# Optimization experiments

Measured on AMD Instinct MI355X. Metric: run time of the kernel, lower is better.

## Reference

```python
import jax, jax.numpy as jnp
import numpy as np

HIDDEN = 2048
N_HEADS = 16
HEAD_DIM = HIDDEN // N_HEADS
ROPE_BASE = 10000.0


def rotate_half(x):
    half = x.shape[-1] // 2
    return jnp.concatenate((-x[..., half:], x[..., :half]), axis=-1)


def rope_cos_sin(seq_len, dtype):
    inv_freq = 1.0 / (ROPE_BASE ** (jnp.arange(0, HEAD_DIM, 2, dtype=jnp.float32) / HEAD_DIM))
    pos = jnp.arange(seq_len, dtype=jnp.float32)
    freqs = jnp.einsum('i,j->ij', pos, inv_freq)  # [S, hd/2]
    emb = jnp.concatenate((freqs, freqs), axis=-1)  # [S, hd]
    return jnp.cos(emb).astype(dtype), jnp.sin(emb).astype(dtype)


def setup_inputs() -> dict:
    key = jax.random.key(0)
    ks = jax.random.split(key, 9)
    B, S, H = 2, 2048, HIDDEN
    std = 1.0 / np.sqrt(H)
    return {
        'hidden_states': jax.random.normal(ks[0], (B, S, H), dtype=jnp.float32),
        'Wq': jax.random.uniform(ks[1], (H, H), jnp.float32, -std, std),
        'bq': jax.random.uniform(ks[2], (H,), jnp.float32, -std, std),
        'Wk': jax.random.uniform(ks[3], (H, H), jnp.float32, -std, std),
        'bk': jax.random.uniform(ks[4], (H,), jnp.float32, -std, std),
        'Wv': jax.random.uniform(ks[5], (H, H), jnp.float32, -std, std),
        'bv': jax.random.uniform(ks[6], (H,), jnp.float32, -std, std),
        'Wo': jax.random.uniform(ks[7], (H, H), jnp.float32, -std, std),
        'bo': jax.random.uniform(ks[8], (H,), jnp.float32, -std, std),
    }


def reference(hidden_states, Wq, bq, Wk, bk, Wv, bv, Wo, bo):
    B, S, H = hidden_states.shape
    scale = HEAD_DIM ** -0.5

    def proj(W, b):
        # torch Linear: x @ W.T + b
        y = jnp.einsum('bsh,oh->bso', hidden_states, W) + b
        return y.reshape(B, S, N_HEADS, HEAD_DIM).transpose(0, 2, 1, 3)  # [B,nh,S,hd]

    q = proj(Wq, bq)
    k = proj(Wk, bk)
    v = proj(Wv, bv)

    cos, sin = rope_cos_sin(S, hidden_states.dtype)  # [S, hd]
    cos = cos[None, None, :, :]
    sin = sin[None, None, :, :]
    q = q * cos + rotate_half(q) * sin
    k = k * cos + rotate_half(k) * sin

    scores = jnp.einsum('bhqd,bhkd->bhqk', q, k) * scale  # [B,nh,S,S]
    probs = jax.nn.softmax(scores, axis=-1)
    ctx = jnp.einsum('bhqk,bhkd->bhqd', probs, v)
    ctx = ctx.transpose(0, 2, 1, 3).reshape(B, S, H)
    return jnp.einsum('bsh,oh->bso', ctx, Wo) + bo
```

## Files before the change

kernel.cpp:

```cpp
#include <hip/hip_runtime.h>
#include <hip/hip_bf16.h>
#include <math.h>

#define HIDDEN 2048
#define NH 16
#define HD 128
#define NB 2
#define SEQ 2048
#define K_DIM 2048

typedef unsigned int u32;
typedef unsigned short ushort_t;
typedef __bf16 bf16x8 __attribute__((ext_vector_type(8)));
typedef float f32x4 __attribute__((ext_vector_type(4)));
typedef ushort_t u16x8 __attribute__((ext_vector_type(8)));

__device__ __forceinline__ void split1(float x, unsigned short& h, unsigned short& l) {
    u32 u = __float_as_uint(x);
    u32 hr = (u + 0x7FFFu + ((u >> 16) & 1u)) >> 16;
    h = (unsigned short)hr;
    float r = x - __uint_as_float(hr << 16);
    u32 u2 = __float_as_uint(r);
    l = (unsigned short)((u2 + 0x7FFFu + ((u2 >> 16) & 1u)) >> 16);
}

__device__ __forceinline__ ushort_t bf16r(float x) {
    u32 u = __float_as_uint(x);
    return (ushort_t)((u + 0x7FFFu + ((u >> 16) & 1u)) >> 16);
}

__device__ __forceinline__ void gl_lds16(const void* g, void* l) {
    __builtin_amdgcn_global_load_lds(
        (const __attribute__((address_space(1))) u32*)g,
        (__attribute__((address_space(3))) u32*)l, 16, 0, 0);
}

__global__ void k_rope_tables(float* __restrict__ ct, float* __restrict__ st) {
    int idx = blockIdx.x * 256 + threadIdx.x;
    int s = idx >> 6, d = idx & 63;
    double inv = pow(10000.0, -(double)d * (1.0 / 64.0));
    double ang = (double)s * inv;
    ct[idx] = (float)cos(ang);
    st[idx] = (float)sin(ang);
}

#define XG 2097152
#define WG 1048576
__global__ void k_cvt_all(const float4* __restrict__ X, const float4* __restrict__ W0,
                          const float4* __restrict__ W1, const float4* __restrict__ W2,
                          ushort4* __restrict__ Xh, ushort4* __restrict__ H0,
                          ushort4* __restrict__ H1, ushort4* __restrict__ H2) {
    int idx = blockIdx.x * 256 + threadIdx.x;
    const float4* src;
    ushort4* dst;
    int off;
    if (idx < XG) { src = X; dst = Xh; off = idx; }
    else {
        int t = idx - XG;
        int m = t >> 20;
        off = t & (WG - 1);
        src = (m == 0) ? W0 : (m == 1) ? W1 : W2;
        dst = (m == 0) ? H0 : (m == 1) ? H1 : H2;
    }
    float4 x = src[off];
    ushort4 h;
    h.x = bf16r(x.x); h.y = bf16r(x.y); h.z = bf16r(x.z); h.w = bf16r(x.w);
    dst[off] = h;
}

__global__ void k_split(const float4* __restrict__ src, ushort4* __restrict__ hi,
                        ushort4* __restrict__ lo) {
    int idx = blockIdx.x * 256 + threadIdx.x;
    float4 x = src[idx];
    ushort4 h, l;
    split1(x.x, h.x, l.x);
    split1(x.y, h.y, l.y);
    split1(x.z, h.z, l.z);
    split1(x.w, h.w, l.w);
    hi[idx] = h;
    lo[idx] = l;
}

#define BAR  __builtin_amdgcn_s_barrier()
#define VM6  asm volatile("s_waitcnt vmcnt(6)" ::: "memory")
#define VM4  asm volatile("s_waitcnt vmcnt(4)" ::: "memory")
#define VM0  asm volatile("s_waitcnt vmcnt(0)" ::: "memory")
#define PRIO1 __builtin_amdgcn_s_setprio(1)
#define PRIO0 __builtin_amdgcn_s_setprio(0)

#define QSTAGE(slot, kt) do { \
    const ushort_t* gA_ = Xh + sgA + (size_t)(kt) * 32; \
    gl_lds16(gA_, &As[slot][(w * 32) * 32]); \
    gl_lds16(gA_ + 16 * 2048, &As[slot][(w * 32 + 16) * 32]); \
    const ushort_t* gB_ = Wsel + sgB + (size_t)(kt) * 32; \
    gl_lds16(gB_, &Bs[slot][(w * 32) * 32]); \
    gl_lds16(gB_ + 16 * 2048, &Bs[slot][(w * 32 + 16) * 32]); \
} while (0)

#define QRD(AD, BD, slot) do { \
    _Pragma("unroll") for (int mf = 0; mf < 8; mf++) \
        AD[mf] = *(const bf16x8*)&As[slot][arow + mf * 512 + ccq]; \
    _Pragma("unroll") for (int nf = 0; nf < 4; nf++) \
        BD[nf] = *(const bf16x8*)&Bs[slot][brow + nf * 512 + ccq]; \
} while (0)

#define QMFMA(AD, BD) do { PRIO1; \
    _Pragma("unroll") for (int mf = 0; mf < 8; mf++) \
    _Pragma("unroll") for (int nf = 0; nf < 4; nf++) \
        acc[mf][nf] = __builtin_amdgcn_mfma_f32_16x16x32_bf16( \
            AD[mf], BD[nf], acc[mf][nf], 0, 0, 0); \
    PRIO0; } while (0)

__global__ __launch_bounds__(512, 2)
void k_gemm_qkv8(const ushort_t* __restrict__ Xh,
                 const ushort_t* __restrict__ W0, const ushort_t* __restrict__ W1,
                 const ushort_t* __restrict__ W2,
                 const float* __restrict__ b0, const float* __restrict__ b1,
                 const float* __restrict__ b2,
                 float* __restrict__ o0, float* __restrict__ o1, float* __restrict__ o2) {
    __shared__ ushort_t As[4][256 * 32];
    __shared__ ushort_t Bs[4][256 * 32];
    const int tid = threadIdx.x;
    const int lane = tid & 63;
    const int w = tid >> 6;
    const int wm = w >> 2;
    const int wn = w & 3;
    const int quad = lane >> 4;
    const int l15 = lane & 15;

    int bid = blockIdx.x;
    bid = (bid & 7) * 48 + (bid >> 3);
    const int bx = bid & 15;
    const int by = bid >> 4;
    const int m0 = bx << 8;
    const int mat = by >> 3;
    const int n0 = (by & 7) << 8;
    const ushort_t* Wsel = (mat == 0) ? W0 : (mat == 1) ? W1 : W2;
    const float* bias = (mat == 0) ? b0 : (mat == 1) ? b1 : b2;
    float* out = (mat == 0) ? o0 : (mat == 1) ? o1 : o2;

    const int lrow4 = lane >> 2;
    const int col8 = (((lane & 3) ^ ((lrow4 >> 1) & 3)) << 3);
    const size_t sgA = (size_t)(m0 + w * 32 + lrow4) * 2048 + col8;
    const size_t sgB = (size_t)(n0 + w * 32 + lrow4) * 2048 + col8;

    const int arow = (wm * 128 + l15) * 32;
    const int brow = (wn * 64 + l15) * 32;
    const int ccq = ((quad ^ ((l15 >> 1) & 3)) << 3);

    f32x4 acc[8][4];
#pragma unroll
    for (int i = 0; i < 8; i++)
#pragma unroll
        for (int j = 0; j < 4; j++) acc[i][j] = (f32x4){0.f, 0.f, 0.f, 0.f};

    bf16x8 aA[8], bA[4], aB[8], bB[4];

    QSTAGE(0, 0); QSTAGE(1, 1);
    VM4; BAR;
    QRD(aA, bA, 0);

    for (int p = 0; p < 60; p += 4) {
        QSTAGE(2, p + 2); VM4; BAR; QRD(aB, bB, 1); QMFMA(aA, bA);
        QSTAGE(3, p + 3); VM4; BAR; QRD(aA, bA, 2); QMFMA(aB, bB);
        QSTAGE(0, p + 4); VM4; BAR; QRD(aB, bB, 3); QMFMA(aA, bA);
        QSTAGE(1, p + 5); VM4; BAR; QRD(aA, bA, 0); QMFMA(aB, bB);
    }
    QSTAGE(2, 62); VM4; BAR; QRD(aB, bB, 1); QMFMA(aA, bA);
    QSTAGE(3, 63); VM4; BAR; QRD(aA, bA, 2); QMFMA(aB, bB);
    VM0; BAR;                QRD(aB, bB, 3); QMFMA(aA, bA);
    QMFMA(aB, bB);

    float bcolv[4];
#pragma unroll
    for (int nf = 0; nf < 4; nf++) bcolv[nf] = bias[n0 + wn * 64 + nf * 16 + l15];

    const int mbase = m0 + wm * 128 + quad * 4;
#pragma unroll
    for (int mf = 0; mf < 8; mf++)
#pragma unroll
        for (int nf = 0; nf < 4; nf++) {
            const int n = n0 + wn * 64 + nf * 16 + l15;
            const int hh = n >> 7;
            const int d = n & 127;
#pragma unroll
            for (int r = 0; r < 4; r++) {
                const int m = mbase + mf * 16 + r;
                const int bb = m >> 11;
                const int s = m & (SEQ - 1);
                out[((size_t)(bb * NH + hh) * SEQ + s) * HD + d] = acc[mf][nf][r] + bcolv[nf];
            }
        }
}

#define OSTAGE(slot, kt) do { \
    const size_t koA = (size_t)((kt) >> 2) * ((size_t)SEQ * HD) + (size_t)((kt) & 3) * 32; \
    const size_t koB = (size_t)(kt) * 32; \
    gl_lds16(Ah + sgA0 + koA, &Ah_s[slot][(w * 32) * 32]); \
    gl_lds16(Ah + sgA0 + 16 * HD + koA, &Ah_s[slot][(w * 32 + 16) * 32]); \
    gl_lds16(Al + sgA0 + koA, &Al_s[slot][(w * 32) * 32]); \
    gl_lds16(Al + sgA0 + 16 * HD + koA, &Al_s[slot][(w * 32 + 16) * 32]); \
    gl_lds16(Bh + sgB0 + koB, &Bh_s[slot][(w * 16) * 32]); \
    gl_lds16(Bl + sgB0 + koB, &Bl_s[slot][(w * 16) * 32]); \
} while (0)

#define ORD(AH, AL, BH, BL, slot) do { \
    _Pragma("unroll") for (int f = 0; f < 4; f++) { \
        AH[f] = *(const bf16x8*)&Ah_s[slot][aro + f * 512 + cco]; \
        AL[f] = *(const bf16x8*)&Al_s[slot][aro + f * 512 + cco]; \
        BH[f] = *(const bf16x8*)&Bh_s[slot][bro + f * 512 + cco]; \
        BL[f] = *(const bf16x8*)&Bl_s[slot][bro + f * 512 + cco]; \
    } \
} while (0)

#define OMFMA(AH, AL, BH, BL) do { PRIO1; \
    _Pragma("unroll") for (int mf = 0; mf < 4; mf++) \
    _Pragma("unroll") for (int nf = 0; nf < 4; nf++) { \
        acc[mf][nf] = __builtin_amdgcn_mfma_f32_16x16x32_bf16( \
            AH[mf], BH[nf], acc[mf][nf], 0, 0, 0); \
        acc[mf][nf] = __builtin_amdgcn_mfma_f32_16x16x32_bf16( \
            AH[mf], BL[nf], acc[mf][nf], 0, 0, 0); \
        acc[mf][nf] = __builtin_amdgcn_mfma_f32_16x16x32_bf16( \
            AL[mf], BH[nf], acc[mf][nf], 0, 0, 0); \
    } PRIO0; } while (0)

__global__ __launch_bounds__(512, 2)
void k_gemm_o2(const ushort_t* __restrict__ Ah, const ushort_t* __restrict__ Al,
               const ushort_t* __restrict__ Bh, const ushort_t* __restrict__ Bl,
               const float* __restrict__ bias, float* __restrict__ out) {
    __shared__ ushort_t Ah_s[3][256 * 32];
    __shared__ ushort_t Al_s[3][256 * 32];
    __shared__ ushort_t Bh_s[3][128 * 32];
    __shared__ ushort_t Bl_s[3][128 * 32];
    const int tid = threadIdx.x;
    const int lane = tid & 63;
    const int w = tid >> 6;
    const int wm = w >> 1;
    const int wn = w & 1;
    const int quad = lane >> 4;
    const int l15 = lane & 15;

    int bid = blockIdx.x;
    bid = (bid & 7) * 32 + (bid >> 3);
    const int bx = bid & 15;
    const int by = bid >> 4;
    const int m0 = bx << 8;
    const int n0 = by << 7;

    const int lrow4 = lane >> 2;
    const int col8 = (((lane & 3) ^ ((lrow4 >> 1) & 3)) << 3);
    const size_t sgA0 = ((size_t)(m0 >> 11) * NH * SEQ + (size_t)((m0 & (SEQ - 1)) + w * 32 + lrow4)) * HD + col8;
    const size_t sgB0 = (size_t)(n0 + w * 16 + lrow4) * K_DIM + col8;

    const int aro = (wm * 64 + l15) * 32;
    const int bro = (wn * 64 + l15) * 32;
    const int cco = ((quad ^ ((l15 >> 1) & 3)) << 3);

    f32x4 acc[4][4];
#pragma unroll
    for (int i = 0; i < 4; i++)
#pragma unroll
        for (int j = 0; j < 4; j++) acc[i][j] = (f32x4){0.f, 0.f, 0.f, 0.f};

    bf16x8 ahA[4], alA[4], bhA[4], blA[4];
    bf16x8 ahB[4], alB[4], bhB[4], blB[4];

    OSTAGE(0, 0);
    OSTAGE(1, 1);
    VM6; BAR;
    ORD(ahA, alA, bhA, blA, 0);

    for (int it = 0; it < 10; ++it) {
        const int q = 6 * it;
        VM0; BAR; OSTAGE(2, q + 2); ORD(ahB, alB, bhB, blB, 1); OMFMA(ahA, alA, bhA, blA);
        VM0; BAR; OSTAGE(0, q + 3); ORD(ahA, alA, bhA, blA, 2); OMFMA(ahB, alB, bhB, blB);
        VM0; BAR; OSTAGE(1, q + 4); ORD(ahB, alB, bhB, blB, 0); OMFMA(ahA, alA, bhA, blA);
        VM0; BAR; OSTAGE(2, q + 5); ORD(ahA, alA, bhA, blA, 1); OMFMA(ahB, alB, bhB, blB);
        VM0; BAR; OSTAGE(0, q + 6); ORD(ahB, alB, bhB, blB, 2); OMFMA(ahA, alA, bhA, blA);
        VM0; BAR; OSTAGE(1, q + 7); ORD(ahA, alA, bhA, blA, 0); OMFMA(ahB, alB, bhB, blB);
    }
    VM0; BAR; OSTAGE(2, 62); ORD(ahB, alB, bhB, blB, 1); OMFMA(ahA, alA, bhA, blA);
    VM0; BAR; OSTAGE(0, 63); ORD(ahA, alA, bhA, blA, 2); OMFMA(ahB, alB, bhB, blB);
    VM0; BAR;                ORD(ahB, alB, bhB, blB, 0); OMFMA(ahA, alA, bhA, blA);
    OMFMA(ahB, alB, bhB, blB);

    float bcolv[4];
#pragma unroll
    for (int nf = 0; nf < 4; nf++) bcolv[nf] = bias[n0 + wn * 64 + nf * 16 + l15];

    const int mb = m0 + wm * 64 + quad * 4;
    const int nb = n0 + wn * 64 + l15;
#pragma unroll
    for (int fm = 0; fm < 4; fm++)
#pragma unroll
        for (int fn = 0; fn < 4; fn++)
#pragma unroll
            for (int r = 0; r < 4; r++)
                out[(size_t)(mb + fm * 16 + r) * HIDDEN + nb + fn * 16] =
                    acc[fm][fn][r] + bcolv[fn];
}

__global__ void k_rope_pack(const float* __restrict__ q, const float* __restrict__ k,
                            const float* __restrict__ ct, const float* __restrict__ st,
                            ushort_t* __restrict__ Qb, ushort_t* __restrict__ Kb) {
    int idx = blockIdx.x * 256 + threadIdx.x;
    int d = idx & 63;
    int s = (idx >> 6) & (SEQ - 1);
    int bh = idx >> 17;
    size_t base = ((size_t)bh * SEQ + s) * HD;
    float c = ct[(s << 6) + d], sn = st[(s << 6) + d];
    const float scq = 0.08838834764831845f;
    float q0 = q[base + d], q1 = q[base + d + 64];
    Qb[base + d]      = bf16r((q0 * c - q1 * sn) * scq);
    Qb[base + d + 64] = bf16r((q1 * c + q0 * sn) * scq);
    float k0 = k[base + d], k1 = k[base + d + 64];
    Kb[base + d]      = bf16r(k0 * c - k1 * sn);
    Kb[base + d + 64] = bf16r(k1 * c + k0 * sn);
}

__global__ __launch_bounds__(256)
void k_vpack(const float* __restrict__ v, ushort_t* __restrict__ vt) {
    __shared__ float t[64][65];
    const int tid = threadIdx.x;
    const int bh = blockIdx.z;
    const int s0 = blockIdx.x << 6;
    const int d0 = blockIdx.y << 6;
    const float* src = v + ((size_t)bh * SEQ + s0) * HD + d0;
    const int rr = tid >> 4;
    const int cc = (tid & 15) << 2;
#pragma unroll
    for (int i = 0; i < 4; i++) {
        float4 x = *(const float4*)(src + (size_t)(i * 16 + rr) * HD + cc);
        t[i * 16 + rr][cc] = x.x;
        t[i * 16 + rr][cc + 1] = x.y;
        t[i * 16 + rr][cc + 2] = x.z;
        t[i * 16 + rr][cc + 3] = x.w;
    }
    __syncthreads();
    const int dr = tid >> 2;
    const int sc_ = (tid & 3) << 4;
    ushort_t* dst = vt + ((size_t)bh * HD + d0 + dr) * SEQ + s0 + sc_;
    u16x8 o0, o1;
#pragma unroll
    for (int u = 0; u < 8; u++) o0[u] = bf16r(t[sc_ + u][dr]);
#pragma unroll
    for (int u = 0; u < 8; u++) o1[u] = bf16r(t[sc_ + 8 + u][dr]);
    *(u16x8*)dst = o0;
    *(u16x8*)(dst + 8) = o1;
}

__global__ __launch_bounds__(256, 2)
void k_flash_mfma(const ushort_t* __restrict__ Qb, const ushort_t* __restrict__ Kb,
                  const ushort_t* __restrict__ Vt,
                  ushort_t* __restrict__ ch, ushort_t* __restrict__ cl) {
    __shared__ ushort_t KV[128 * 136];
    __shared__ ushort_t Ps[128 * 136];
    const int tid = threadIdx.x;
    const int lane = tid & 63;
    const int w = tid >> 6;
    const int quad = lane >> 4;
    const int l15 = lane & 15;
    const int bi = blockIdx.x;
    const int bh = bi & 31;
    const int qt = bi >> 5;
    const ushort_t* Qg = Qb + ((size_t)bh * SEQ + ((size_t)qt << 7)) * HD;
    const ushort_t* Kg = Kb + (size_t)bh * SEQ * HD;
    const ushort_t* Vg = Vt + (size_t)bh * HD * SEQ;

    bf16x8 qf[2][4];
#pragma unroll
    for (int qi = 0; qi < 2; qi++)
#pragma unroll
        for (int ks = 0; ks < 4; ks++)
            qf[qi][ks] = *(const bf16x8*)(Qg + (size_t)(w * 32 + qi * 16 + l15) * HD + ks * 32 + quad * 8);

    const int sr = tid >> 4;
    const int sc8 = (tid & 15) << 3;

    u16x8 Kreg[8], Vreg[8];
#pragma unroll
    for (int i = 0; i < 8; i++)
        Kreg[i] = *(const u16x8*)(Kg + (size_t)(i * 16 + sr) * HD + sc8);
#pragma unroll
    for (int i = 0; i < 8; i++)
        Vreg[i] = *(const u16x8*)(Vg + (size_t)(i * 16 + sr) * SEQ + sc8);

    f32x4 acc[2][8];
#pragma unroll
    for (int qi = 0; qi < 2; qi++)
#pragma unroll
        for (int d = 0; d < 8; d++) acc[qi][d] = (f32x4){0.f, 0.f, 0.f, 0.f};
    float lp[2] = {0.f, 0.f};

    for (int kt = 0; kt < SEQ; kt += 128) {
        const int np = kt + 128;
        __syncthreads();
#pragma unroll
        for (int i = 0; i < 8; i++)
            *(u16x8*)&KV[(i * 16 + sr) * 136 + sc8] = Kreg[i];
        if (np < SEQ) {
#pragma unroll
            for (int i = 0; i < 8; i++)
                Kreg[i] = *(const u16x8*)(Kg + (size_t)(np + i * 16 + sr) * HD + sc8);
        }
        __syncthreads();

        f32x4 sc[2][8];
#pragma unroll
        for (int qi = 0; qi < 2; qi++)
#pragma unroll
            for (int j = 0; j < 8; j++) sc[qi][j] = (f32x4){0.f, 0.f, 0.f, 0.f};
#pragma unroll
        for (int ks = 0; ks < 4; ks++) {
#pragma unroll
            for (int jh = 0; jh < 2; jh++) {
                bf16x8 kf[4];
#pragma unroll
                for (int j = 0; j < 4; j++)
                    kf[j] = *(const bf16x8*)&KV[((jh * 4 + j) * 16 + l15) * 136 + ks * 32 + quad * 8];
#pragma unroll
                for (int qi = 0; qi < 2; qi++)
#pragma unroll
                    for (int j = 0; j < 4; j++)
                        sc[qi][jh * 4 + j] = __builtin_amdgcn_mfma_f32_16x16x32_bf16(
                            kf[j], qf[qi][ks], sc[qi][jh * 4 + j], 0, 0, 0);
            }
        }

#pragma unroll
        for (int qi = 0; qi < 2; qi++) {
            const int prow = (w * 32 + qi * 16 + l15) * 136 + quad * 4;
#pragma unroll
            for (int j = 0; j < 8; j++) {
                float p0 = __expf(sc[qi][j][0]);
                float p1 = __expf(sc[qi][j][1]);
                float p2 = __expf(sc[qi][j][2]);
                float p3 = __expf(sc[qi][j][3]);
                lp[qi] += (p0 + p1) + (p2 + p3);
                __hip_bfloat162 lo2 = __float22bfloat162_rn({p0, p1});
                __hip_bfloat162 hi2 = __float22bfloat162_rn({p2, p3});
                uint2 pk = make_uint2(*(u32*)&lo2, *(u32*)&hi2);
                *(uint2*)&Ps[prow + j * 16] = pk;
            }
        }
        __syncthreads();
#pragma unroll
        for (int i = 0; i < 8; i++)
            *(u16x8*)&KV[(i * 16 + sr) * 136 + sc8] = Vreg[i];
        if (np < SEQ) {
#pragma unroll
            for (int i = 0; i < 8; i++)
                Vreg[i] = *(const u16x8*)(Vg + (size_t)(i * 16 + sr) * SEQ + np + sc8);
        }
        __syncthreads();

#pragma unroll
        for (int ks = 0; ks < 4; ks++) {
            bf16x8 pf[2];
#pragma unroll
            for (int qi = 0; qi < 2; qi++)
                pf[qi] = *(const bf16x8*)&Ps[(w * 32 + qi * 16 + l15) * 136 + ks * 32 + quad * 8];
#pragma unroll
            for (int db = 0; db < 8; db++) {
                bf16x8 vf = *(const bf16x8*)&KV[(db * 16 + l15) * 136 + ks * 32 + quad * 8];
#pragma unroll
                for (int qi = 0; qi < 2; qi++)
                    acc[qi][db] = __builtin_amdgcn_mfma_f32_16x16x32_bf16(vf, pf[qi], acc[qi][db], 0, 0, 0);
            }
        }
    }

    float inv[2];
#pragma unroll
    for (int qi = 0; qi < 2; qi++) {
        float l = lp[qi];
        l += __shfl_xor(l, 16);
        l += __shfl_xor(l, 32);
        inv[qi] = 1.0f / l;
    }
    const size_t obase = ((size_t)bh * SEQ + ((size_t)qt << 7)) * HD;

    __syncthreads();
#pragma unroll
    for (int qi = 0; qi < 2; qi++)
#pragma unroll
        for (int db = 0; db < 8; db++) {
            ushort4 hh;
            ushort_t dum;
            split1(acc[qi][db][0] * inv[qi], hh.x, dum);
            split1(acc[qi][db][1] * inv[qi], hh.y, dum);
            split1(acc[qi][db][2] * inv[qi], hh.z, dum);
            split1(acc[qi][db][3] * inv[qi], hh.w, dum);
            *(ushort4*)&Ps[(w * 32 + qi * 16 + l15) * 136 + db * 16 + quad * 4] = hh;
        }
    __syncthreads();
#pragma unroll
    for (int t = 0; t < 8; t++) {
        int c = t * 256 + tid;
        int row = c >> 4, col8 = (c & 15) << 3;
        *(u16x8*)&ch[obase + (size_t)row * HD + col8] = *(const u16x8*)&Ps[row * 136 + col8];
    }
    __syncthreads();
#pragma unroll
    for (int qi = 0; qi < 2; qi++)
#pragma unroll
        for (int db = 0; db < 8; db++) {
            ushort4 ll;
            ushort_t dum;
            split1(acc[qi][db][0] * inv[qi], dum, ll.x);
            split1(acc[qi][db][1] * inv[qi], dum, ll.y);
            split1(acc[qi][db][2] * inv[qi], dum, ll.z);
            split1(acc[qi][db][3] * inv[qi], dum, ll.w);
            *(ushort4*)&Ps[(w * 32 + qi * 16 + l15) * 136 + db * 16 + quad * 4] = ll;
        }
    __syncthreads();
#pragma unroll
    for (int t = 0; t < 8; t++) {
        int c = t * 256 + tid;
        int row = c >> 4, col8 = (c & 15) << 3;
        *(u16x8*)&cl[obase + (size_t)row * HD + col8] = *(const u16x8*)&Ps[row * 136 + col8];
    }
}

extern "C" void kernel_launch(void* const* d_in, const int* in_sizes, int n_in,
                              void* d_out, int out_size, void* d_ws, size_t ws_size,
                              hipStream_t stream) {
    const float* X  = (const float*)d_in[0];
    const float* Wq = (const float*)d_in[1];
    const float* bq = (const float*)d_in[2];
    const float* Wk = (const float*)d_in[3];
    const float* bk = (const float*)d_in[4];
    const float* Wv = (const float*)d_in[5];
    const float* bv = (const float*)d_in[6];
    const float* Wo = (const float*)d_in[7];
    const float* bo = (const float*)d_in[8];
    float* out = (float*)d_out;

    const size_t QS = (size_t)NB * NH * SEQ * HD;
    const size_t WS = (size_t)HIDDEN * HIDDEN;
    float* q_ws = (float*)d_ws;
    float* k_ws = q_ws + QS;
    float* v_ws = k_ws + QS;
    float* cost = v_ws + QS;
    float* sint = cost + (size_t)SEQ * 64;
    ushort_t* Xh = (ushort_t*)(sint + (size_t)SEQ * 64);
    ushort_t* Wh0 = Xh + QS;
    ushort_t* Wh1 = Wh0 + WS;
    ushort_t* Wh2 = Wh1 + WS;
    ushort_t* Woh = Wh2 + WS;
    ushort_t* Wol = Woh + WS;
    ushort_t* Kb  = Wol + WS;
    ushort_t* Vtb = Kb + QS;
    ushort_t* ctxh = (ushort_t*)q_ws;
    ushort_t* ctxl = ctxh + QS;

    k_rope_tables<<<(SEQ * 64) / 256, 256, 0, stream>>>(cost, sint);

    k_cvt_all<<<(XG + 3 * WG) / 256, 256, 0, stream>>>(
        (const float4*)X, (const float4*)Wq, (const float4*)Wk, (const float4*)Wv,
        (ushort4*)Xh, (ushort4*)Wh0, (ushort4*)Wh1, (ushort4*)Wh2);
    k_split<<<WS / 4 / 256, 256, 0, stream>>>((const float4*)Wo, (ushort4*)Woh, (ushort4*)Wol);

    k_gemm_qkv8<<<384, 512, 0, stream>>>(Xh, Wh0, Wh1, Wh2, bq, bk, bv,
                                         q_ws, k_ws, v_ws);

    ushort_t* Qbb = Xh;
    k_rope_pack<<<(NB * NH * SEQ * 64) / 256, 256, 0, stream>>>(q_ws, k_ws, cost, sint, Qbb, Kb);
    k_vpack<<<dim3(SEQ / 64, HD / 64, NB * NH), 256, 0, stream>>>(v_ws, Vtb);

    k_flash_mfma<<<512, 256, 0, stream>>>(Qbb, Kb, Vtb, ctxh, ctxl);

    k_gemm_o2<<<256, 512, 0, stream>>>(ctxh, ctxl, Woh, Wol, bo, out);
}
```

Before: 513.8 us.

## Store QKV projections as bf16 and merge small conversion and packing kernels

The QKV GEMM epilogue now writes bf16 instead of fp32, which halves the intermediate traffic consumed by the RoPE and V-transpose stages. The separate Wo split kernel is folded into the conversion kernel, and the RoPE pack and V pack kernels are merged into one launch, cutting launch count. This adds one extra bf16 rounding of q/k/v before RoPE, a small accuracy change relative to the fp32 intermediate.

```diff
diff --git a/kernel.cpp b/kernel.cpp
--- a/kernel.cpp
+++ b/kernel.cpp
@@ -29,6 +29,10 @@
     return (ushort_t)((u + 0x7FFFu + ((u >> 16) & 1u)) >> 16);
 }
 
+__device__ __forceinline__ float bf2f(ushort_t u) {
+    return __uint_as_float(((u32)u) << 16);
+}
+
 __device__ __forceinline__ void gl_lds16(const void* g, void* l) {
     __builtin_amdgcn_global_load_lds(
         (const __attribute__((address_space(1))) u32*)g,
@@ -48,37 +52,38 @@
 #define WG 1048576
 __global__ void k_cvt_all(const float4* __restrict__ X, const float4* __restrict__ W0,
                           const float4* __restrict__ W1, const float4* __restrict__ W2,
+                          const float4* __restrict__ Wo,
                           ushort4* __restrict__ Xh, ushort4* __restrict__ H0,
-                          ushort4* __restrict__ H1, ushort4* __restrict__ H2) {
+                          ushort4* __restrict__ H1, ushort4* __restrict__ H2,
+                          ushort4* __restrict__ WoH, ushort4* __restrict__ WoL) {
     int idx = blockIdx.x * 256 + threadIdx.x;
-    const float4* src;
-    ushort4* dst;
-    int off;
-    if (idx < XG) { src = X; dst = Xh; off = idx; }
-    else {
-        int t = idx - XG;
-        int m = t >> 20;
-        off = t & (WG - 1);
-        src = (m == 0) ? W0 : (m == 1) ? W1 : W2;
-        dst = (m == 0) ? H0 : (m == 1) ? H1 : H2;
-    }
-    float4 x = src[off];
-    ushort4 h;
-    h.x = bf16r(x.x); h.y = bf16r(x.y); h.z = bf16r(x.z); h.w = bf16r(x.w);
-    dst[off] = h;
-}
-
-__global__ void k_split(const float4* __restrict__ src, ushort4* __restrict__ hi,
-                        ushort4* __restrict__ lo) {
-    int idx = blockIdx.x * 256 + threadIdx.x;
-    float4 x = src[idx];
-    ushort4 h, l;
-    split1(x.x, h.x, l.x);
-    split1(x.y, h.y, l.y);
-    split1(x.z, h.z, l.z);
-    split1(x.w, h.w, l.w);
-    hi[idx] = h;
-    lo[idx] = l;
+    if (idx < XG + 3 * WG) {
+        const float4* src;
+        ushort4* dst;
+        int off;
+        if (idx < XG) { src = X; dst = Xh; off = idx; }
+        else {
+            int t = idx - XG;
+            int m = t >> 20;
+            off = t & (WG - 1);
+            src = (m == 0) ? W0 : (m == 1) ? W1 : W2;
+            dst = (m == 0) ? H0 : (m == 1) ? H1 : H2;
+        }
+        float4 x = src[off];
+        ushort4 h;
+        h.x = bf16r(x.x); h.y = bf16r(x.y); h.z = bf16r(x.z); h.w = bf16r(x.w);
+        dst[off] = h;
+    } else {
+        int off = idx - XG - 3 * WG;
+        float4 x = Wo[off];
+        ushort4 h, l;
+        split1(x.x, h.x, l.x);
+        split1(x.y, h.y, l.y);
+        split1(x.z, h.z, l.z);
+        split1(x.w, h.w, l.w);
+        WoH[off] = h;
+        WoL[off] = l;
+    }
 }
 
 #define BAR  __builtin_amdgcn_s_barrier()
@@ -117,7 +122,8 @@
                  const ushort_t* __restrict__ W2,
                  const float* __restrict__ b0, const float* __restrict__ b1,
                  const float* __restrict__ b2,
-                 float* __restrict__ o0, float* __restrict__ o1, float* __restrict__ o2) {
+                 ushort_t* __restrict__ o0, ushort_t* __restrict__ o1,
+                 ushort_t* __restrict__ o2) {
     __shared__ ushort_t As[4][256 * 32];
     __shared__ ushort_t Bs[4][256 * 32];
     const int tid = threadIdx.x;
@@ -137,7 +143,7 @@
     const int n0 = (by & 7) << 8;
     const ushort_t* Wsel = (mat == 0) ? W0 : (mat == 1) ? W1 : W2;
     const float* bias = (mat == 0) ? b0 : (mat == 1) ? b1 : b2;
-    float* out = (mat == 0) ? o0 : (mat == 1) ? o1 : o2;
+    ushort_t* out = (mat == 0) ? o0 : (mat == 1) ? o1 : o2;
 
     const int lrow4 = lane >> 2;
     const int col8 = (((lane & 3) ^ ((lrow4 >> 1) & 3)) << 3);
@@ -188,7 +194,8 @@
                 const int m = mbase + mf * 16 + r;
                 const int bb = m >> 11;
                 const int s = m & (SEQ - 1);
-                out[((size_t)(bb * NH + hh) * SEQ + s) * HD + d] = acc[mf][nf][r] + bcolv[nf];
+                out[((size_t)(bb * NH + hh) * SEQ + s) * HD + d] =
+                    bf16r(acc[mf][nf][r] + bcolv[nf]);
             }
         }
 }
@@ -300,53 +307,57 @@
                     acc[fm][fn][r] + bcolv[fn];
 }
 
-__global__ void k_rope_pack(const float* __restrict__ q, const float* __restrict__ k,
-                            const float* __restrict__ ct, const float* __restrict__ st,
-                            ushort_t* __restrict__ Qb, ushort_t* __restrict__ Kb) {
-    int idx = blockIdx.x * 256 + threadIdx.x;
-    int d = idx & 63;
-    int s = (idx >> 6) & (SEQ - 1);
-    int bh = idx >> 17;
-    size_t base = ((size_t)bh * SEQ + s) * HD;
-    float c = ct[(s << 6) + d], sn = st[(s << 6) + d];
-    const float scq = 0.08838834764831845f;
-    float q0 = q[base + d], q1 = q[base + d + 64];
-    Qb[base + d]      = bf16r((q0 * c - q1 * sn) * scq);
-    Qb[base + d + 64] = bf16r((q1 * c + q0 * sn) * scq);
-    float k0 = k[base + d], k1 = k[base + d + 64];
-    Kb[base + d]      = bf16r(k0 * c - k1 * sn);
-    Kb[base + d + 64] = bf16r(k1 * c + k0 * sn);
-}
-
 __global__ __launch_bounds__(256)
-void k_vpack(const float* __restrict__ v, ushort_t* __restrict__ vt) {
+void k_rope_vpack(const ushort_t* __restrict__ qb, const ushort_t* __restrict__ kb,
+                  const ushort_t* __restrict__ vb,
+                  const float* __restrict__ ct, const float* __restrict__ st,
+                  ushort_t* __restrict__ Qb, ushort_t* __restrict__ Kb,
+                  ushort_t* __restrict__ vt) {
     __shared__ float t[64][65];
     const int tid = threadIdx.x;
-    const int bh = blockIdx.z;
-    const int s0 = blockIdx.x << 6;
-    const int d0 = blockIdx.y << 6;
-    const float* src = v + ((size_t)bh * SEQ + s0) * HD + d0;
-    const int rr = tid >> 4;
-    const int cc = (tid & 15) << 2;
-#pragma unroll
-    for (int i = 0; i < 4; i++) {
-        float4 x = *(const float4*)(src + (size_t)(i * 16 + rr) * HD + cc);
-        t[i * 16 + rr][cc] = x.x;
-        t[i * 16 + rr][cc + 1] = x.y;
-        t[i * 16 + rr][cc + 2] = x.z;
-        t[i * 16 + rr][cc + 3] = x.w;
-    }
-    __syncthreads();
-    const int dr = tid >> 2;
-    const int sc_ = (tid & 3) << 4;
-    ushort_t* dst = vt + ((size_t)bh * HD + d0 + dr) * SEQ + s0 + sc_;
-    u16x8 o0, o1;
-#pragma unroll
-    for (int u = 0; u < 8; u++) o0[u] = bf16r(t[sc_ + u][dr]);
-#pragma unroll
-    for (int u = 0; u < 8; u++) o1[u] = bf16r(t[sc_ + 8 + u][dr]);
-    *(u16x8*)dst = o0;
-    *(u16x8*)(dst + 8) = o1;
+    const int blk = blockIdx.x;
+    if (blk < 16384) {
+        int idx = blk * 256 + tid;
+        int d = idx & 63;
+        int s = (idx >> 6) & (SEQ - 1);
+        int bh = idx >> 17;
+        size_t base = ((size_t)bh * SEQ + s) * HD;
+        float c = ct[(s << 6) + d], sn = st[(s << 6) + d];
+        const float scq = 0.08838834764831845f;
+        float q0 = bf2f(qb[base + d]), q1 = bf2f(qb[base + d + 64]);
+        Qb[base + d]      = bf16r((q0 * c - q1 * sn) * scq);
+        Qb[base + d + 64] = bf16r((q1 * c + q0 * sn) * scq);
+        float k0 = bf2f(kb[base + d]), k1 = bf2f(kb[base + d + 64]);
+        Kb[base + d]      = bf16r(k0 * c - k1 * sn);
+        Kb[base + d + 64] = bf16r(k1 * c + k0 * sn);
+    } else {
+        int b = blk - 16384;
+        const int s0 = (b & 31) << 6;
+        const int d0 = ((b >> 5) & 1) << 6;
+        const int bh = b >> 6;
+        const ushort_t* src = vb + ((size_t)bh * SEQ + s0) * HD + d0;
+        const int rr = tid >> 4;
+        const int cc = (tid & 15) << 2;
+#pragma unroll
+        for (int i = 0; i < 4; i++) {
+            ushort4 x = *(const ushort4*)(src + (size_t)(i * 16 + rr) * HD + cc);
+            t[i * 16 + rr][cc]     = bf2f(x.x);
+            t[i * 16 + rr][cc + 1] = bf2f(x.y);
+            t[i * 16 + rr][cc + 2] = bf2f(x.z);
+            t[i * 16 + rr][cc + 3] = bf2f(x.w);
+        }
+        __syncthreads();
+        const int dr = tid >> 2;
+        const int sc_ = (tid & 3) << 4;
+        ushort_t* dst = vt + ((size_t)bh * HD + d0 + dr) * SEQ + s0 + sc_;
+        u16x8 o0, o1;
+#pragma unroll
+        for (int u = 0; u < 8; u++) o0[u] = bf16r(t[sc_ + u][dr]);
+#pragma unroll
+        for (int u = 0; u < 8; u++) o1[u] = bf16r(t[sc_ + 8 + u][dr]);
+        *(u16x8*)dst = o0;
+        *(u16x8*)(dst + 8) = o1;
+    }
 }
 
 __global__ __launch_bounds__(256, 2)
@@ -495,8 +506,8 @@
         }
     __syncthreads();
 #pragma unroll
-    for (int t = 0; t < 8; t++) {
-        int c = t * 256 + tid;
+    for (int t2 = 0; t2 < 8; t2++) {
+        int c = t2 * 256 + tid;
         int row = c >> 4, col8 = (c & 15) << 3;
         *(u16x8*)&ch[obase + (size_t)row * HD + col8] = *(const u16x8*)&Ps[row * 136 + col8];
     }
@@ -515,8 +526,8 @@
         }
     __syncthreads();
 #pragma unroll
-    for (int t = 0; t < 8; t++) {
-        int c = t * 256 + tid;
+    for (int t2 = 0; t2 < 8; t2++) {
+        int c = t2 * 256 + tid;
         int row = c >> 4, col8 = (c & 15) << 3;
         *(u16x8*)&cl[obase + (size_t)row * HD + col8] = *(const u16x8*)&Ps[row * 136 + col8];
     }
@@ -538,10 +549,10 @@
 
     const size_t QS = (size_t)NB * NH * SEQ * HD;
     const size_t WS = (size_t)HIDDEN * HIDDEN;
-    float* q_ws = (float*)d_ws;
-    float* k_ws = q_ws + QS;
-    float* v_ws = k_ws + QS;
-    float* cost = v_ws + QS;
+    ushort_t* qb_ws = (ushort_t*)d_ws;
+    ushort_t* kb_ws = qb_ws + QS;
+    ushort_t* vb_ws = kb_ws + QS;
+    float* cost = (float*)(vb_ws + QS);
     float* sint = cost + (size_t)SEQ * 64;
     ushort_t* Xh = (ushort_t*)(sint + (size_t)SEQ * 64);
     ushort_t* Wh0 = Xh + QS;
@@ -551,24 +562,25 @@
     ushort_t* Wol = Woh + WS;
     ushort_t* Kb  = Wol + WS;
     ushort_t* Vtb = Kb + QS;
-    ushort_t* ctxh = (ushort_t*)q_ws;
-    ushort_t* ctxl = ctxh + QS;
+    ushort_t* ctxh = qb_ws;
+    ushort_t* ctxl = kb_ws;
 
     k_rope_tables<<<(SEQ * 64) / 256, 256, 0, stream>>>(cost, sint);
 
-    k_cvt_all<<<(XG + 3 * WG) / 256, 256, 0, stream>>>(
+    k_cvt_all<<<(XG + 4 * WG) / 256, 256, 0, stream>>>(
         (const float4*)X, (const float4*)Wq, (const float4*)Wk, (const float4*)Wv,
-        (ushort4*)Xh, (ushort4*)Wh0, (ushort4*)Wh1, (ushort4*)Wh2);
-    k_split<<<WS / 4 / 256, 256, 0, stream>>>((const float4*)Wo, (ushort4*)Woh, (ushort4*)Wol);
+        (const float4*)Wo,
+        (ushort4*)Xh, (ushort4*)Wh0, (ushort4*)Wh1, (ushort4*)Wh2,
+        (ushort4*)Woh, (ushort4*)Wol);
 
     k_gemm_qkv8<<<384, 512, 0, stream>>>(Xh, Wh0, Wh1, Wh2, bq, bk, bv,
-                                         q_ws, k_ws, v_ws);
+                                         qb_ws, kb_ws, vb_ws);
 
     ushort_t* Qbb = Xh;
-    k_rope_pack<<<(NB * NH * SEQ * 64) / 256, 256, 0, stream>>>(q_ws, k_ws, cost, sint, Qbb, Kb);
-    k_vpack<<<dim3(SEQ / 64, HD / 64, NB * NH), 256, 0, stream>>>(v_ws, Vtb);
+    k_rope_vpack<<<16384 + 2048, 256, 0, stream>>>(qb_ws, kb_ws, vb_ws, cost, sint,
+                                                   Qbb, Kb, Vtb);
 
     k_flash_mfma<<<512, 256, 0, stream>>>(Qbb, Kb, Vtb, ctxh, ctxl);
 
-    k_gemm_o2<<<256, 512, 0, stream>>>(ctxh, ctxl, Woh, Wol, bo, out);
-}
+    k_gemm_o2<<<dim3(256), 512, 0, stream>>>(ctxh, ctxl, Woh, Wol, bo, out);
+}
```

Result: faster. 501.7 us (-2.4%).
